# Kernel tuning notes

Hardware: AMD Instinct MI355X
Metric: run time of the kernel (lower is better)

The kernel has to match this reference:

```python
import jax, jax.numpy as jnp
import numpy as np

N = 50000       # nodes per side
E = 800000      # edges per side
F_IN = 64       # num_node_features
H = 96          # embeding_size
G = 256         # number of graphs in batch


def _param(key, shape, scale=0.05):
    return scale * jax.random.normal(key, shape, dtype=jnp.float32)


def setup_inputs() -> dict:
    key = jax.random.key(0)
    ks = jax.random.split(key, 32)
    inp = {
        "x_p": jax.random.normal(ks[0], (N, F_IN), dtype=jnp.float32),
        "x_d": jax.random.normal(ks[1], (N, F_IN), dtype=jnp.float32),
        "edge_attr_p": jax.random.normal(ks[2], (E, 8), dtype=jnp.float32),
        "edge_attr_d": jax.random.normal(ks[3], (E, 8), dtype=jnp.float32),
        "edge_index_p": jax.random.randint(ks[4], (2, E), 0, N, dtype=jnp.int32),
        "edge_index_d": jax.random.randint(ks[5], (2, E), 0, N, dtype=jnp.int32),
        "x_p_batch": jnp.sort(jax.random.randint(ks[6], (N,), 0, G, dtype=jnp.int32)),
        "x_d_batch": jnp.sort(jax.random.randint(ks[7], (N,), 0, G, dtype=jnp.int32)),
        # GCNConv stacks (first layer F_IN->H, then H->H)
        "Wp0": _param(ks[8], (F_IN, H)), "bp0": jnp.zeros((H,), jnp.float32),
        "Wp1": _param(ks[9], (H, H)),    "bp1": jnp.zeros((H,), jnp.float32),
        "Wp2": _param(ks[10], (H, H)),   "bp2": jnp.zeros((H,), jnp.float32),
        "Wd0": _param(ks[11], (F_IN, H)), "bd0": jnp.zeros((H,), jnp.float32),
        "Wd1": _param(ks[12], (H, H)),    "bd1": jnp.zeros((H,), jnp.float32),
        "Wd2": _param(ks[13], (H, H)),    "bd2": jnp.zeros((H,), jnp.float32),
        # GlobalAttention gate MLP: Linear(F_IN,F_IN) -> ReLU -> Linear(F_IN,1)
        "gW1": _param(ks[14], (F_IN, F_IN)), "gb1": jnp.zeros((F_IN,), jnp.float32),
        "gW2": _param(ks[15], (F_IN, 1)),    "gb2": jnp.zeros((1,), jnp.float32),
        # final MLP: Linear(2H+2F_IN, H) -> ReLU -> Linear(H, 1)
        "lW0": _param(ks[16], (2 * H + 2 * F_IN, H)), "lb0": jnp.zeros((H,), jnp.float32),
        "lW1": _param(ks[17], (H, 1)),                "lb1": jnp.zeros((1,), jnp.float32),
    }
    return inp


def gcn_conv(x, W, b, src, dst, dinv):
    # PyG GCNConv: x' = D^{-1/2} (A + I) D^{-1/2} (x W) + b
    xw = x @ W                                              # [N, H]
    norm = dinv[src] * dinv[dst]                            # [E]
    agg = jax.ops.segment_sum(norm[:, None] * xw[src], dst, num_segments=x.shape[0])
    agg = agg + (dinv * dinv)[:, None] * xw                 # self-loop term
    return agg + b


def deg_inv_sqrt(dst, n):
    deg = jax.ops.segment_sum(jnp.ones(dst.shape, jnp.float32), dst, num_segments=n) + 1.0
    return deg ** -0.5


def att_pool(x, batch, gW1, gb1, gW2, gb2):
    # GlobalAttention: softmax(gate_nn(x)) per graph, weighted sum of x
    gate = (jnp.maximum(x @ gW1 + gb1, 0.0) @ gW2 + gb2)[:, 0]     # [N]
    m = jax.ops.segment_max(gate, batch, num_segments=G)
    e = jnp.exp(gate - m[batch])
    denom = jax.ops.segment_sum(e, batch, num_segments=G)
    alpha = e / denom[batch]
    return jax.ops.segment_sum(alpha[:, None] * x, batch, num_segments=G)  # [G, F]


def mean_pool(x, batch):
    s = jax.ops.segment_sum(x, batch, num_segments=G)
    cnt = jax.ops.segment_sum(jnp.ones((x.shape[0],), jnp.float32), batch, num_segments=G)
    return s / jnp.maximum(cnt, 1.0)[:, None]


def reference(x_p, x_d, edge_attr_p, edge_attr_d, edge_index_p, edge_index_d,
              x_p_batch, x_d_batch,
              Wp0, bp0, Wp1, bp1, Wp2, bp2,
              Wd0, bd0, Wd1, bd1, Wd2, bd2,
              gW1, gb1, gW2, gb2, lW0, lb0, lW1, lb1):
    src_p, dst_p = edge_index_p[0], edge_index_p[1]
    src_d, dst_d = edge_index_d[0], edge_index_d[1]

    # attention pooling on raw node features (attention=True)
    x_p_att = att_pool(x_p, x_p_batch, gW1, gb1, gW2, gb2)
    x_d_att = att_pool(x_d, x_d_batch, gW1, gb1, gW2, gb2)

    dinv_p = deg_inv_sqrt(dst_p, N)
    dinv_d = deg_inv_sqrt(dst_d, N)

    hp = jnp.maximum(gcn_conv(x_p, Wp0, bp0, src_p, dst_p, dinv_p), 0.0)
    hp = jnp.maximum(gcn_conv(hp, Wp1, bp1, src_p, dst_p, dinv_p), 0.0)
    hp = gcn_conv(hp, Wp2, bp2, src_p, dst_p, dinv_p)

    hd = jnp.maximum(gcn_conv(x_d, Wd0, bd0, src_d, dst_d, dinv_d), 0.0)
    hd = jnp.maximum(gcn_conv(hd, Wd1, bd1, src_d, dst_d, dinv_d), 0.0)
    hd = gcn_conv(hd, Wd2, bd2, src_d, dst_d, dinv_d)

    xp = mean_pool(hp, x_p_batch)   # [G, H]
    xd = mean_pool(hd, x_d_batch)   # [G, H]

    x = jnp.concatenate([xp, xd, x_p_att, x_d_att], axis=1)  # [G, 2H+2F]
    # dropout p=0.5 is identity in eval mode
    x = jnp.maximum(x @ lW0 + lb0, 0.0)
    x = x @ lW1 + lb1               # [G, 1]
    return x
```

## Files before the change

### kernel.cpp

```cpp
#include <hip/hip_runtime.h>

#define NN 50000
#define NE 800000
#define FIN 64
#define HH 96
#define NG 256
#define NB ((NN + 255) / 256)
#define NPB 196
#define NCB 256
#define BA 256
#define EPB (NE / BA)
#define CAPA 48
#define CAPB 3584

__device__ __forceinline__ float wave_sum(float v) {
    #pragma unroll
    for (int off = 32; off > 0; off >>= 1) v += __shfl_down(v, off, 64);
    return v;
}
__device__ __forceinline__ float wave_max(float v) {
    #pragma unroll
    for (int off = 32; off > 0; off >>= 1) v = fmaxf(v, __shfl_down(v, off, 64));
    return v;
}
__device__ __forceinline__ float bf2f(unsigned short b) {
    return __uint_as_float(((unsigned int)b) << 16);
}
__device__ __forceinline__ unsigned short f2bf(float f) {
    unsigned int u = __float_as_uint(f);
    u += 0x7FFFu + ((u >> 16) & 1u);
    return (unsigned short)(u >> 16);
}

__global__ __launch_bounds__(256) void permuteA(const int* __restrict__ srcP,
                                                const int* __restrict__ dstP,
                                                const int* __restrict__ srcD,
                                                const int* __restrict__ dstD,
                                                unsigned int* __restrict__ tmpP,
                                                unsigned int* __restrict__ tmpD,
                                                int* __restrict__ cntA) {
    __shared__ int cnt[NCB];
    __shared__ unsigned int stage[NCB][CAPA];
    int t = threadIdx.x, blk = blockIdx.x, side = blockIdx.y;
    const int* src = side ? srcD : srcP;
    const int* dst = side ? dstD : dstP;
    unsigned int* tmp = side ? tmpD : tmpP;
    cnt[t] = 0;
    __syncthreads();
    int e0 = blk * EPB;
    for (int i = t; i < EPB; i += 256) {
        int s = src[e0 + i], d = dst[e0 + i];
        int b = d / NPB;
        int ld = d - b * NPB;
        int slot = atomicAdd(&cnt[b], 1);
        if (slot < CAPA)
            stage[b][slot] = ((unsigned int)s << 8) | (unsigned int)ld;
    }
    __syncthreads();
    for (int idx = t; idx < NCB * CAPA; idx += 256) {
        int b = idx / CAPA, j = idx - b * CAPA;
        if (j < cnt[b])
            tmp[((size_t)blk * NCB + b) * CAPA + j] = stage[b][j];
    }
    cntA[(side * BA + blk) * NCB + t] = min(cnt[t], CAPA);
}

__global__ __launch_bounds__(256) void bucket_scan(const int* __restrict__ cntA,
                                                   int* __restrict__ bucketBase) {
    int side = blockIdx.x, t = threadIdx.x;
    __shared__ int sc[NCB];
    __shared__ int tot_s[NCB];
    int tot = 0;
    for (int blk = 0; blk < BA; ++blk)
        tot += cntA[(side * BA + blk) * NCB + t];
    tot_s[t] = tot; sc[t] = tot;
    __syncthreads();
    for (int off = 1; off < NCB; off <<= 1) {
        int v = (t >= off) ? sc[t - off] : 0;
        __syncthreads();
        sc[t] += v;
        __syncthreads();
    }
    bucketBase[side * (NCB + 1) + t] = sc[t] - tot_s[t];
    if (t == NCB - 1) bucketBase[side * (NCB + 1) + NCB] = sc[t];
}

__global__ __launch_bounds__(256) void permuteB(const unsigned int* __restrict__ tmpP,
                                                const unsigned int* __restrict__ tmpD,
                                                const int* __restrict__ cntA,
                                                const int* __restrict__ bucketBase,
                                                int* __restrict__ rowptr2,
                                                float* __restrict__ dinv2,
                                                int* __restrict__ eSrcP,
                                                int* __restrict__ eSrcD) {
    __shared__ int segLen[BA];
    __shared__ int hist[256];
    __shared__ int sc[256];
    __shared__ int cursor[NPB];
    __shared__ int srcStage[CAPB];
    int b = blockIdx.x, side = blockIdx.y, t = threadIdx.x;
    const unsigned int* tmp = side ? tmpD : tmpP;
    int* eS = side ? eSrcD : eSrcP;
    segLen[t] = cntA[(side * BA + t) * NCB + b];
    hist[t] = 0;
    __syncthreads();
    for (int idx = t; idx < BA * CAPA; idx += 256) {
        int blk = idx / CAPA, j = idx - blk * CAPA;
        if (j < segLen[blk])
            atomicAdd(&hist[tmp[((size_t)blk * NCB + b) * CAPA + j] & 255], 1);
    }
    __syncthreads();
    sc[t] = hist[t];
    __syncthreads();
    for (int off = 1; off < 256; off <<= 1) {
        int v = (t >= off) ? sc[t - off] : 0;
        __syncthreads();
        sc[t] += v;
        __syncthreads();
    }
    int excl = sc[t] - hist[t];
    int TB = sc[255];
    int GB = bucketBase[side * (NCB + 1) + b];
    int node0 = b * NPB;
    if (t < NPB && node0 + t < NN) {
        rowptr2[side * (NN + 1) + node0 + t] = GB + excl;
        dinv2[side * NN + node0 + t] = rsqrtf((float)hist[t] + 1.0f);
        cursor[t] = excl;
    }
    if (b == NCB - 1 && t == 0) rowptr2[side * (NN + 1) + NN] = GB + TB;
    __syncthreads();
    for (int idx = t; idx < BA * CAPA; idx += 256) {
        int blk = idx / CAPA, j = idx - blk * CAPA;
        if (j < segLen[blk]) {
            unsigned int r = tmp[((size_t)blk * NCB + b) * CAPA + j];
            int pos = atomicAdd(&cursor[r & 255], 1);
            srcStage[pos] = (int)(r >> 8);
        }
    }
    __syncthreads();
    for (int i = t; i < TB; i += 256) eS[GB + i] = srcStage[i];
}

__global__ __launch_bounds__(256) void start_both(const int* __restrict__ batchP,
                                                  const int* __restrict__ batchD,
                                                  int* __restrict__ start2) {
    int i = blockIdx.x * 256 + threadIdx.x;
    if (i >= NN) return;
    int side = blockIdx.y;
    const int* batch = side ? batchD : batchP;
    int* start = start2 + side * (NG + 1);
    int b = batch[i];
    int prev = (i == 0) ? -1 : batch[i - 1];
    for (int g = prev + 1; g <= b; ++g) start[g] = i;
    if (i == NN - 1) {
        for (int g = b + 1; g <= NG; ++g) start[g] = NN;
    }
}

__global__ __launch_bounds__(256) void gate_both(const float* __restrict__ xP,
                                                 const float* __restrict__ xD,
                                                 const float* __restrict__ gW1,
                                                 const float* __restrict__ gb1,
                                                 const float* __restrict__ gW2,
                                                 const float* __restrict__ gb2,
                                                 float* __restrict__ gate2) {
    __shared__ float w1[64 * 64];
    __shared__ float b1v[64], w2v[64];
    __shared__ float partial[256];
    int side = blockIdx.y;
    const float* x = side ? xD : xP;
    float* gate = gate2 + side * NN;
    int t = threadIdx.x;
    int node = blockIdx.x * 64 + (t & 63);
    int q = t >> 6;
    for (int idx = t; idx < 64 * 64; idx += 256) w1[idx] = gW1[idx];
    if (t < 64) { b1v[t] = gb1[t]; w2v[t] = gW2[t]; }
    __syncthreads();

    float xr[64];
    if (node < NN) {
        #pragma unroll
        for (int k4 = 0; k4 < 64; k4 += 4) {
            float4 v = *reinterpret_cast<const float4*>(x + (size_t)node * 64 + k4);
            xr[k4] = v.x; xr[k4 + 1] = v.y; xr[k4 + 2] = v.z; xr[k4 + 3] = v.w;
        }
    } else {
        #pragma unroll
        for (int k = 0; k < 64; ++k) xr[k] = 0.0f;
    }
    float hid[16];
    #pragma unroll
    for (int j = 0; j < 16; ++j) hid[j] = b1v[q * 16 + j];
    for (int k = 0; k < 64; ++k) {
        float xv = xr[k];
        #pragma unroll
        for (int j = 0; j < 16; ++j) hid[j] += xv * w1[k * 64 + q * 16 + j];
    }
    float acc = 0.0f;
    #pragma unroll
    for (int j = 0; j < 16; ++j) acc += fmaxf(hid[j], 0.0f) * w2v[q * 16 + j];
    partial[t] = acc;
    __syncthreads();
    if (t < 64 && node < NN)
        gate[node] = partial[t] + partial[64 + t] + partial[128 + t] + partial[192 + t] + gb2[0];
}

template <int K, bool RELU>
__global__ __launch_bounds__(256) void gemm_both(const float* __restrict__ inP,
                                                 const float* __restrict__ inD,
                                                 const float* __restrict__ WP,
                                                 const float* __restrict__ WD,
                                                 ushort4* __restrict__ xwP,
                                                 ushort4* __restrict__ xwD) {
    __shared__ float wlds[K * HH];
    int t = threadIdx.x;
    int side = blockIdx.y;
    const float* x = side ? inD : inP;
    const float* W = side ? WD : WP;
    ushort4* xw = side ? xwD : xwP;
    for (int idx = t; idx < K * HH; idx += 256) wlds[idx] = W[idx];
    __syncthreads();

    int n = blockIdx.x * 256 + t;
    if (n >= NN) return;
    float xr[K];
    #pragma unroll
    for (int k4 = 0; k4 < K; k4 += 4) {
        float4 v = *reinterpret_cast<const float4*>(x + (size_t)n * K + k4);
        if (RELU) {
            v.x = fmaxf(v.x, 0.0f); v.y = fmaxf(v.y, 0.0f);
            v.z = fmaxf(v.z, 0.0f); v.w = fmaxf(v.w, 0.0f);
        }
        xr[k4] = v.x; xr[k4 + 1] = v.y; xr[k4 + 2] = v.z; xr[k4 + 3] = v.w;
    }
    #pragma unroll
    for (int c = 0; c < HH; c += 4) {
        float a0 = 0.f, a1 = 0.f, a2 = 0.f, a3 = 0.f;
        #pragma unroll
        for (int k = 0; k < K; ++k) {
            float4 w = *reinterpret_cast<const float4*>(&wlds[k * HH + c]);
            a0 += xr[k] * w.x; a1 += xr[k] * w.y;
            a2 += xr[k] * w.z; a3 += xr[k] * w.w;
        }
        ushort4 o;
        o.x = f2bf(a0); o.y = f2bf(a1); o.z = f2bf(a2); o.w = f2bf(a3);
        xw[n * 24 + (c >> 2)] = o;
    }
}

__global__ __launch_bounds__(256) void gather_both(const ushort4* __restrict__ xwP,
                                                   const ushort4* __restrict__ xwD,
                                                   const float* __restrict__ dinv2,
                                                   const float* __restrict__ biasP,
                                                   const float* __restrict__ biasD,
                                                   const int* __restrict__ rowptr2,
                                                   const int* __restrict__ eSrcP,
                                                   const int* __restrict__ eSrcD,
                                                   float* __restrict__ aggP,
                                                   float* __restrict__ aggD) {
    int i = blockIdx.x * 256 + threadIdx.x;
    if (i >= NN * 24) return;
    int side = blockIdx.y;
    const ushort4* xw = side ? xwD : xwP;
    const float* dv = dinv2 + side * NN;
    const float* bias = side ? biasD : biasP;
    const int* rp = rowptr2 + side * (NN + 1);
    const int* es = side ? eSrcD : eSrcP;
    float* agg = side ? aggD : aggP;

    int n = i / 24, q = i - n * 24;
    int r0 = rp[n], r1 = rp[n + 1];
    float ex = 0.f, ey = 0.f, ez = 0.f, ew = 0.f;
    int r = r0;
    for (; r + 2 <= r1; r += 2) {
        int s0 = es[r], s1 = es[r + 1];
        float w0 = dv[s0], w1 = dv[s1];
        ushort4 u0 = xw[s0 * 24 + q];
        ushort4 u1 = xw[s1 * 24 + q];
        ex += w0 * bf2f(u0.x) + w1 * bf2f(u1.x);
        ey += w0 * bf2f(u0.y) + w1 * bf2f(u1.y);
        ez += w0 * bf2f(u0.z) + w1 * bf2f(u1.z);
        ew += w0 * bf2f(u0.w) + w1 * bf2f(u1.w);
    }
    if (r < r1) {
        int s0 = es[r];
        float w0 = dv[s0];
        ushort4 u0 = xw[s0 * 24 + q];
        ex += w0 * bf2f(u0.x); ey += w0 * bf2f(u0.y);
        ez += w0 * bf2f(u0.z); ew += w0 * bf2f(u0.w);
    }
    float d = dv[n], d2 = d * d;
    ushort4 su = xw[i];
    float4 b = reinterpret_cast<const float4*>(bias)[q];
    float4 o;
    o.x = d2 * bf2f(su.x) + d * ex + b.x;
    o.y = d2 * bf2f(su.y) + d * ey + b.y;
    o.z = d2 * bf2f(su.z) + d * ez + b.z;
    o.w = d2 * bf2f(su.w) + d * ew + b.w;
    reinterpret_cast<float4*>(agg)[i] = o;
}

__global__ __launch_bounds__(256) void pool_ab_wgt(const float* __restrict__ gate2,
                                                   const int* __restrict__ start2,
                                                   float* __restrict__ den2,
                                                   float* __restrict__ wgt2) {
    int side = blockIdx.y, g = blockIdx.x, t = threadIdx.x;
    const float* gate = gate2 + side * NN;
    const int* start = start2 + side * (NG + 1);
    float* den = den2 + side * NG;
    float* wgt = wgt2 + side * NN;
    int s = start[g], e = start[g + 1];
    __shared__ float red[4];
    __shared__ float s_m;

    float lm = -3.0e38f;
    for (int i = s + t; i < e; i += 256) lm = fmaxf(lm, gate[i]);
    lm = wave_max(lm);
    if ((t & 63) == 0) red[t >> 6] = lm;
    __syncthreads();
    if (t == 0) s_m = fmaxf(fmaxf(red[0], red[1]), fmaxf(red[2], red[3]));
    __syncthreads();
    float m = s_m;

    float ls = 0.0f;
    for (int i = s + t; i < e; i += 256) {
        float w = expf(gate[i] - m);
        wgt[i] = w;
        ls += w;
    }
    ls = wave_sum(ls);
    __syncthreads();
    if ((t & 63) == 0) red[t >> 6] = ls;
    __syncthreads();
    if (t == 0) den[g] = red[0] + red[1] + red[2] + red[3];
}

__global__ __launch_bounds__(256) void pool_att_both(const float* __restrict__ wgt2,
                                                     const float* __restrict__ xP,
                                                     const float* __restrict__ xD,
                                                     const int* __restrict__ batchP,
                                                     const int* __restrict__ batchD,
                                                     float* __restrict__ attP,
                                                     float* __restrict__ attD) {
    int side = blockIdx.y;
    const float* w = wgt2 + side * NN;
    const float* x = side ? xD : xP;
    const int* batch = side ? batchD : batchP;
    float* attRaw = side ? attD : attP;
    int base = blockIdx.x * 64;
    int t = threadIdx.x;
    int f = t & 63, sub = t >> 6;
    float acc = 0.0f;
    int cur = -1;
    for (int j = 0; j < 16; ++j) {
        int i = base + sub + j * 4;
        if (i >= NN) break;
        int g = batch[i];
        if (g != cur) {
            if (cur >= 0) atomicAdd(&attRaw[cur * FIN + f], acc);
            cur = g; acc = 0.0f;
        }
        acc += w[i] * x[(size_t)i * FIN + f];
    }
    if (cur >= 0) atomicAdd(&attRaw[cur * FIN + f], acc);
}

__global__ __launch_bounds__(256) void pool_mean_both(const float* __restrict__ hP,
                                                      const float* __restrict__ hD,
                                                      const int* __restrict__ batchP,
                                                      const int* __restrict__ batchD,
                                                      float* __restrict__ meanP,
                                                      float* __restrict__ meanD) {
    int t = threadIdx.x;
    if (t >= 240) return;
    int side = blockIdx.y;
    const float* h = side ? hD : hP;
    const int* batch = side ? batchD : batchP;
    float* meanRaw = side ? meanD : meanP;
    int q = t % 24, sub = t / 24;
    int base = blockIdx.x * 80;
    float4 acc = {0.f, 0.f, 0.f, 0.f};
    int cur = -1;
    for (int j = 0; j < 8; ++j) {
        int i = base + sub + j * 10;
        if (i >= NN) continue;
        int g = batch[i];
        if (g != cur) {
            if (cur >= 0) {
                float* o = meanRaw + cur * HH + q * 4;
                atomicAdd(o + 0, acc.x); atomicAdd(o + 1, acc.y);
                atomicAdd(o + 2, acc.z); atomicAdd(o + 3, acc.w);
            }
            cur = g; acc.x = acc.y = acc.z = acc.w = 0.f;
        }
        float4 v = reinterpret_cast<const float4*>(h)[(size_t)i * 24 + q];
        acc.x += v.x; acc.y += v.y; acc.z += v.z; acc.w += v.w;
    }
    if (cur >= 0) {
        float* o = meanRaw + cur * HH + q * 4;
        atomicAdd(o + 0, acc.x); atomicAdd(o + 1, acc.y);
        atomicAdd(o + 2, acc.z); atomicAdd(o + 3, acc.w);
    }
}

__global__ __launch_bounds__(128) void final_mlp(const float* __restrict__ meanP,
                                                 const float* __restrict__ meanD,
                                                 const float* __restrict__ attP,
                                                 const float* __restrict__ attD,
                                                 const float* __restrict__ den2,
                                                 const int* __restrict__ start2,
                                                 const float* __restrict__ lW0,
                                                 const float* __restrict__ lb0,
                                                 const float* __restrict__ lW1,
                                                 const float* __restrict__ lb1,
                                                 float* __restrict__ out) {
    __shared__ float in[2 * HH + 2 * FIN];
    __shared__ float red[2];
    int g = blockIdx.x, t = threadIdx.x;
    const int* startP = start2;
    const int* startD = start2 + (NG + 1);
    float cP = fmaxf((float)(startP[g + 1] - startP[g]), 1.0f);
    float cD = fmaxf((float)(startD[g + 1] - startD[g]), 1.0f);
    float dP = den2[g], dD = den2[NG + g];
    for (int idx = t; idx < 320; idx += 128) {
        float v;
        if (idx < 96)       v = meanP[g * HH + idx] / cP;
        else if (idx < 192) v = meanD[g * HH + idx - 96] / cD;
        else if (idx < 256) v = (dP > 0.f) ? attP[g * FIN + idx - 192] / dP : 0.0f;
        else                v = (dD > 0.f) ? attD[g * FIN + idx - 256] / dD : 0.0f;
        in[idx] = v;
    }
    __syncthreads();
    float hidv = 0.0f;
    if (t < HH) {
        float acc = lb0[t];
        for (int k = 0; k < 320; ++k) acc += in[k] * lW0[k * HH + t];
        hidv = fmaxf(acc, 0.0f) * lW1[t];
    }
    float v = wave_sum(hidv);
    if ((t & 63) == 0) red[t >> 6] = v;
    __syncthreads();
    if (t == 0) out[g] = red[0] + red[1] + lb1[0];
}

extern "C" void kernel_launch(void* const* d_in, const int* in_sizes, int n_in,
                              void* d_out, int out_size, void* d_ws, size_t ws_size,
                              hipStream_t stream) {
    const float* x_p = (const float*)d_in[0];
    const float* x_d = (const float*)d_in[1];
    const int* ei_p = (const int*)d_in[4];
    const int* ei_d = (const int*)d_in[5];
    const int* batch_p = (const int*)d_in[6];
    const int* batch_d = (const int*)d_in[7];
    const float* Wp0 = (const float*)d_in[8];  const float* bp0 = (const float*)d_in[9];
    const float* Wp1 = (const float*)d_in[10]; const float* bp1 = (const float*)d_in[11];
    const float* Wp2 = (const float*)d_in[12]; const float* bp2 = (const float*)d_in[13];
    const float* Wd0 = (const float*)d_in[14]; const float* bd0 = (const float*)d_in[15];
    const float* Wd1 = (const float*)d_in[16]; const float* bd1 = (const float*)d_in[17];
    const float* Wd2 = (const float*)d_in[18]; const float* bd2 = (const float*)d_in[19];
    const float* gW1 = (const float*)d_in[20]; const float* gb1 = (const float*)d_in[21];
    const float* gW2 = (const float*)d_in[22]; const float* gb2 = (const float*)d_in[23];
    const float* lW0 = (const float*)d_in[24]; const float* lb0 = (const float*)d_in[25];
    const float* lW1 = (const float*)d_in[26]; const float* lb1 = (const float*)d_in[27];

    const int* src_p = ei_p;        const int* dst_p = ei_p + NE;
    const int* src_d = ei_d;        const int* dst_d = ei_d + NE;

    char* ws = (char*)d_ws;
    size_t off = 0;
    auto alloc = [&](size_t bytes) -> void* {
        void* p = ws + off;
        off = (off + bytes + 255) & ~(size_t)255;
        return p;
    };
    float* agg_p = (float*)alloc((size_t)NN * HH * 4);
    float* agg_d = (float*)alloc((size_t)NN * HH * 4);
    ushort4* xw_p = (ushort4*)alloc((size_t)NN * HH * 2);
    ushort4* xw_d = (ushort4*)alloc((size_t)NN * HH * 2);
    float* dinv2 = (float*)alloc((size_t)2 * NN * 4);
    int* rowptr2 = (int*)alloc((size_t)2 * (NN + 1) * 4);
    int* eSrc_p = (int*)alloc((size_t)NE * 4);
    int* eSrc_d = (int*)alloc((size_t)NE * 4);
    float* gate2 = (float*)alloc((size_t)2 * NN * 4);
    float* wgt2 = (float*)alloc((size_t)2 * NN * 4);
    int* start2 = (int*)alloc((size_t)2 * (NG + 1) * 4);
    float* den2 = (float*)alloc((size_t)2 * NG * 4);
    int* cntA = (int*)alloc((size_t)2 * BA * NCB * 4);
    int* bucketBase = (int*)alloc((size_t)2 * (NCB + 1) * 4);
    float* pooled = (float*)alloc((size_t)NG * (2 * HH + 2 * FIN) * 4);
    float* meanP = pooled;
    float* meanD = meanP + (size_t)NG * HH;
    float* attP  = meanD + (size_t)NG * HH;
    float* attD  = attP + (size_t)NG * FIN;
    unsigned int* tmp_p = (unsigned int*)agg_p;
    unsigned int* tmp_d = (unsigned int*)agg_d;
    (void)ws_size; (void)n_in; (void)in_sizes; (void)out_size;

    const int BNV = (NN * 24 + 255) / 256;
    const dim3 G2N(NB, 2), G2V(BNV, 2);
    const dim3 GEMM_GRID(NB, 2);
    const dim3 GATE_GRID((NN + 63) / 64, 2);
    const dim3 GAB(NG, 2);
    const dim3 GATT((NN + 63) / 64, 2);
    const dim3 GMEAN((NN + 79) / 80, 2);

    hipMemsetAsync(pooled, 0, (size_t)NG * (2 * HH + 2 * FIN) * 4, stream);

    permuteA<<<dim3(BA, 2), 256, 0, stream>>>(src_p, dst_p, src_d, dst_d, tmp_p, tmp_d, cntA);
    bucket_scan<<<2, 256, 0, stream>>>(cntA, bucketBase);
    permuteB<<<dim3(NCB, 2), 256, 0, stream>>>(tmp_p, tmp_d, cntA, bucketBase,
                                               rowptr2, dinv2, eSrc_p, eSrc_d);
    start_both<<<G2N, 256, 0, stream>>>(batch_p, batch_d, start2);
    gate_both<<<GATE_GRID, 256, 0, stream>>>(x_p, x_d, gW1, gb1, gW2, gb2, gate2);
    pool_ab_wgt<<<GAB, 256, 0, stream>>>(gate2, start2, den2, wgt2);
    pool_att_both<<<GATT, 256, 0, stream>>>(wgt2, x_p, x_d, batch_p, batch_d, attP, attD);

    gemm_both<FIN, false><<<GEMM_GRID, 256, 0, stream>>>(x_p, x_d, Wp0, Wd0, xw_p, xw_d);
    gather_both<<<G2V, 256, 0, stream>>>(xw_p, xw_d, dinv2, bp0, bd0, rowptr2, eSrc_p, eSrc_d, agg_p, agg_d);
    gemm_both<HH, true><<<GEMM_GRID, 256, 0, stream>>>(agg_p, agg_d, Wp1, Wd1, xw_p, xw_d);
    gather_both<<<G2V, 256, 0, stream>>>(xw_p, xw_d, dinv2, bp1, bd1, rowptr2, eSrc_p, eSrc_d, agg_p, agg_d);
    gemm_both<HH, true><<<GEMM_GRID, 256, 0, stream>>>(agg_p, agg_d, Wp2, Wd2, xw_p, xw_d);
    gather_both<<<G2V, 256, 0, stream>>>(xw_p, xw_d, dinv2, bp2, bd2, rowptr2, eSrc_p, eSrc_d, agg_p, agg_d);
    pool_mean_both<<<GMEAN, 256, 0, stream>>>(agg_p, agg_d, batch_p, batch_d, meanP, meanD);

    final_mlp<<<NG, 128, 0, stream>>>(meanP, meanD, attP, attD, den2, start2,
                                      lW0, lb0, lW1, lb1, (float*)d_out);
}
```

Measured before the change: 629.9 us.

## Store GCN intermediate features as FP8 E4M3 and split GEMM columns

The per-layer XW features are now stored as software-encoded FP8 (E4M3) instead of bf16, halving the bytes fetched by the random-access neighbour gather. The GEMM kernel also splits its 96 output columns across two blocks in a new grid dimension, halving the shared-memory weight tile and doubling block count. The trade-off is a large precision loss in intermediate features, plus extra ALU work for software encode and decode, with branches on every element. The x rows are also read twice by the GEMM.

```diff
diff --git a/kernel.cpp b/kernel.cpp
--- a/kernel.cpp
+++ b/kernel.cpp
@@ -23,13 +23,31 @@
     for (int off = 32; off > 0; off >>= 1) v = fmaxf(v, __shfl_down(v, off, 64));
     return v;
 }
-__device__ __forceinline__ float bf2f(unsigned short b) {
-    return __uint_as_float(((unsigned int)b) << 16);
-}
-__device__ __forceinline__ unsigned short f2bf(float f) {
-    unsigned int u = __float_as_uint(f);
-    u += 0x7FFFu + ((u >> 16) & 1u);
-    return (unsigned short)(u >> 16);
+__device__ __forceinline__ float fp82f(unsigned char b) {
+    unsigned int em = b & 0x7Fu;
+    float mag;
+    if (em >= 8u) {
+        unsigned int u = (((em >> 3) + 120u) << 23) | ((em & 7u) << 20);
+        mag = __uint_as_float(u);
+    } else {
+        mag = (float)em * 0x1.0p-9f;
+    }
+    return (b & 0x80u) ? -mag : mag;
+}
+__device__ __forceinline__ unsigned char f2fp8(float f) {
+    unsigned int bits = __float_as_uint(f);
+    unsigned char s = (unsigned char)((bits >> 24) & 0x80u);
+    float a = fabsf(f);
+    if (a >= 448.0f) return s | 0x7E;
+    if (a < 0x1.0p-6f) {
+        int m = (int)rintf(a * 512.0f);
+        return s | (unsigned char)m;
+    }
+    unsigned int u = __float_as_uint(a);
+    u += 0x7FFFFu + ((u >> 20) & 1u);
+    unsigned int exp = (u >> 23) - 127u + 7u;
+    unsigned int man = (u >> 20) & 7u;
+    return s | (unsigned char)((exp << 3) | man);
 }
 
 __global__ __launch_bounds__(256) void permuteA(const int* __restrict__ srcP,
@@ -210,15 +228,19 @@
                                                  const float* __restrict__ inD,
                                                  const float* __restrict__ WP,
                                                  const float* __restrict__ WD,
-                                                 ushort4* __restrict__ xwP,
-                                                 ushort4* __restrict__ xwD) {
-    __shared__ float wlds[K * HH];
+                                                 uchar4* __restrict__ xwP,
+                                                 uchar4* __restrict__ xwD) {
+    __shared__ float wlds[K * 48];
     int t = threadIdx.x;
-    int side = blockIdx.y;
+    int side = blockIdx.z;
+    int c0 = blockIdx.y * 48;
     const float* x = side ? inD : inP;
     const float* W = side ? WD : WP;
-    ushort4* xw = side ? xwD : xwP;
-    for (int idx = t; idx < K * HH; idx += 256) wlds[idx] = W[idx];
+    uchar4* xw = side ? xwD : xwP;
+    for (int idx = t; idx < K * 48; idx += 256) {
+        int k = idx / 48, c = idx - k * 48;
+        wlds[idx] = W[k * HH + c0 + c];
+    }
     __syncthreads();
 
     int n = blockIdx.x * 256 + t;
@@ -234,22 +256,22 @@
         xr[k4] = v.x; xr[k4 + 1] = v.y; xr[k4 + 2] = v.z; xr[k4 + 3] = v.w;
     }
     #pragma unroll
-    for (int c = 0; c < HH; c += 4) {
+    for (int c = 0; c < 48; c += 4) {
         float a0 = 0.f, a1 = 0.f, a2 = 0.f, a3 = 0.f;
         #pragma unroll
         for (int k = 0; k < K; ++k) {
-            float4 w = *reinterpret_cast<const float4*>(&wlds[k * HH + c]);
+            float4 w = *reinterpret_cast<const float4*>(&wlds[k * 48 + c]);
             a0 += xr[k] * w.x; a1 += xr[k] * w.y;
             a2 += xr[k] * w.z; a3 += xr[k] * w.w;
         }
-        ushort4 o;
-        o.x = f2bf(a0); o.y = f2bf(a1); o.z = f2bf(a2); o.w = f2bf(a3);
-        xw[n * 24 + (c >> 2)] = o;
-    }
-}
-
-__global__ __launch_bounds__(256) void gather_both(const ushort4* __restrict__ xwP,
-                                                   const ushort4* __restrict__ xwD,
+        uchar4 o;
+        o.x = f2fp8(a0); o.y = f2fp8(a1); o.z = f2fp8(a2); o.w = f2fp8(a3);
+        xw[n * 24 + ((c0 + c) >> 2)] = o;
+    }
+}
+
+__global__ __launch_bounds__(256) void gather_both(const uchar4* __restrict__ xwP,
+                                                   const uchar4* __restrict__ xwD,
                                                    const float* __restrict__ dinv2,
                                                    const float* __restrict__ biasP,
                                                    const float* __restrict__ biasD,
@@ -261,7 +283,7 @@
     int i = blockIdx.x * 256 + threadIdx.x;
     if (i >= NN * 24) return;
     int side = blockIdx.y;
-    const ushort4* xw = side ? xwD : xwP;
+    const uchar4* xw = side ? xwD : xwP;
     const float* dv = dinv2 + side * NN;
     const float* bias = side ? biasD : biasP;
     const int* rp = rowptr2 + side * (NN + 1);
@@ -275,28 +297,28 @@
     for (; r + 2 <= r1; r += 2) {
         int s0 = es[r], s1 = es[r + 1];
         float w0 = dv[s0], w1 = dv[s1];
-        ushort4 u0 = xw[s0 * 24 + q];
-        ushort4 u1 = xw[s1 * 24 + q];
-        ex += w0 * bf2f(u0.x) + w1 * bf2f(u1.x);
-        ey += w0 * bf2f(u0.y) + w1 * bf2f(u1.y);
-        ez += w0 * bf2f(u0.z) + w1 * bf2f(u1.z);
-        ew += w0 * bf2f(u0.w) + w1 * bf2f(u1.w);
+        uchar4 u0 = xw[s0 * 24 + q];
+        uchar4 u1 = xw[s1 * 24 + q];
+        ex += w0 * fp82f(u0.x) + w1 * fp82f(u1.x);
+        ey += w0 * fp82f(u0.y) + w1 * fp82f(u1.y);
+        ez += w0 * fp82f(u0.z) + w1 * fp82f(u1.z);
+        ew += w0 * fp82f(u0.w) + w1 * fp82f(u1.w);
     }
     if (r < r1) {
         int s0 = es[r];
         float w0 = dv[s0];
-        ushort4 u0 = xw[s0 * 24 + q];
-        ex += w0 * bf2f(u0.x); ey += w0 * bf2f(u0.y);
-        ez += w0 * bf2f(u0.z); ew += w0 * bf2f(u0.w);
+        uchar4 u0 = xw[s0 * 24 + q];
+        ex += w0 * fp82f(u0.x); ey += w0 * fp82f(u0.y);
+        ez += w0 * fp82f(u0.z); ew += w0 * fp82f(u0.w);
     }
     float d = dv[n], d2 = d * d;
-    ushort4 su = xw[i];
+    uchar4 su = xw[i];
     float4 b = reinterpret_cast<const float4*>(bias)[q];
     float4 o;
-    o.x = d2 * bf2f(su.x) + d * ex + b.x;
-    o.y = d2 * bf2f(su.y) + d * ey + b.y;
-    o.z = d2 * bf2f(su.z) + d * ez + b.z;
-    o.w = d2 * bf2f(su.w) + d * ew + b.w;
+    o.x = d2 * fp82f(su.x) + d * ex + b.x;
+    o.y = d2 * fp82f(su.y) + d * ey + b.y;
+    o.z = d2 * fp82f(su.z) + d * ez + b.z;
+    o.w = d2 * fp82f(su.w) + d * ew + b.w;
     reinterpret_cast<float4*>(agg)[i] = o;
 }
 
@@ -475,8 +497,8 @@
     };
     float* agg_p = (float*)alloc((size_t)NN * HH * 4);
     float* agg_d = (float*)alloc((size_t)NN * HH * 4);
-    ushort4* xw_p = (ushort4*)alloc((size_t)NN * HH * 2);
-    ushort4* xw_d = (ushort4*)alloc((size_t)NN * HH * 2);
+    uchar4* xw_p = (uchar4*)alloc((size_t)NN * HH);
+    uchar4* xw_d = (uchar4*)alloc((size_t)NN * HH);
     float* dinv2 = (float*)alloc((size_t)2 * NN * 4);
     int* rowptr2 = (int*)alloc((size_t)2 * (NN + 1) * 4);
     int* eSrc_p = (int*)alloc((size_t)NE * 4);
@@ -498,7 +520,7 @@
 
     const int BNV = (NN * 24 + 255) / 256;
     const dim3 G2N(NB, 2), G2V(BNV, 2);
-    const dim3 GEMM_GRID(NB, 2);
+    const dim3 GEMM_GRID(NB, 2, 2);
     const dim3 GATE_GRID((NN + 63) / 64, 2);
     const dim3 GAB(NG, 2);
     const dim3 GATT((NN + 63) / 64, 2);
```

After: 975.8 us. +54.9%, slower.
